# Performance work log

Measured on AMD Instinct MI355X. Metric: run time of the kernel, lower is better.

## Reference

```python
import jax, jax.numpy as jnp
import numpy as np

HEADS = 16
DIM_HEAD = 64
QUERY_DIM = 1024
CONTEXT_DIM = 1024
D_ATTN = HEADS * DIM_HEAD
SCALE = DIM_HEAD ** -0.5


def setup_inputs() -> dict:
    key = jax.random.key(0)
    ks = jax.random.split(key, 7)
    B, N, M = 4, 2048, 1024
    x = jax.random.normal(ks[0], (B, N, QUERY_DIM), dtype=jnp.float32)
    context = jax.random.normal(ks[1], (B, M, CONTEXT_DIM), dtype=jnp.float32)
    # Linear weights stored as [in, out] (no bias for Q/K/V, bias for to_out)
    s = 0.02
    Wq = jax.random.normal(ks[2], (QUERY_DIM, D_ATTN), dtype=jnp.float32) * s
    Wk = jax.random.normal(ks[3], (CONTEXT_DIM, D_ATTN), dtype=jnp.float32) * s
    Wv = jax.random.normal(ks[4], (CONTEXT_DIM, D_ATTN), dtype=jnp.float32) * s
    Wo = jax.random.normal(ks[5], (D_ATTN, QUERY_DIM), dtype=jnp.float32) * s
    bo = jax.random.normal(ks[6], (QUERY_DIM,), dtype=jnp.float32) * s
    return {"x": x, "context": context, "Wq": Wq, "Wk": Wk, "Wv": Wv, "Wo": Wo, "bo": bo}


def reference(x, context, Wq, Wk, Wv, Wo, bo):
    B, N, _ = x.shape
    M = context.shape[1]
    Q = (x @ Wq).reshape(B, N, HEADS, DIM_HEAD)        # b n h d
    K = (context @ Wk).reshape(B, M, HEADS, DIM_HEAD)  # b m h d
    V = (context @ Wv).reshape(B, M, HEADS, DIM_HEAD)
    # scores: b q h m  (matches torch einsum 'bqhd,bhmd->bqhm')
    scores = jnp.einsum('bqhd,bmhd->bqhm', Q, K) * SCALE
    attn = jax.nn.softmax(scores, axis=-1)
    out = jnp.einsum('bqhm,bmhd->bqhd', attn, V)
    out = out.reshape(B, N, D_ATTN)
    return out @ Wo + bo  # dropout p=0.0 -> identity
```

## Files before the change

kernel.cpp:

```cpp
#include <hip/hip_runtime.h>
#include <math.h>


#define HEADS 16
#define DHEAD 64
#define DM    1024
#define BQ    4
#define NQ    2048
#define MK    1024

typedef unsigned short u16;
typedef __attribute__((ext_vector_type(8))) short bf16x8;
typedef __attribute__((ext_vector_type(4))) float f32x4;
typedef __attribute__((ext_vector_type(16))) float f32x16;

__device__ __forceinline__ u16 f2bf(float f) {
  unsigned u = __builtin_bit_cast(unsigned, f);
  u = u + 0x7FFFu + ((u >> 16) & 1u);
  return (u16)(u >> 16);
}

__device__ __forceinline__ unsigned cvtpk(float lo, float hi2) {
  unsigned r;
  asm("v_cvt_pk_bf16_f32 %0, %1, %2" : "=v"(r) : "v"(lo), "v"(hi2));
  return r;
}

__device__ __forceinline__ float max3f(float a, float b, float c) {
  float d;
  asm("v_max3_f32 %0, %1, %2, %3" : "=v"(d) : "v"(a), "v"(b), "v"(c));
  return d;
}

__device__ __forceinline__ void gld16(const u16* g, u16* l) {
  __builtin_amdgcn_global_load_lds((const __attribute__((address_space(1))) void*)g,
                                   (__attribute__((address_space(3))) void*)l,
                                   16, 0, 0);
}

__global__ void k_cvt(const float* __restrict__ in, u16* __restrict__ out, int n8) {
  int i = blockIdx.x * 256 + threadIdx.x;
  if (i >= n8) return;
  float4 a = ((const float4*)in)[i * 2];
  float4 b = ((const float4*)in)[i * 2 + 1];
  union { u16 h[8]; int4 v; } r;
  r.h[0] = f2bf(a.x); r.h[1] = f2bf(a.y); r.h[2] = f2bf(a.z); r.h[3] = f2bf(a.w);
  r.h[4] = f2bf(b.x); r.h[5] = f2bf(b.y); r.h[6] = f2bf(b.z); r.h[7] = f2bf(b.w);
  ((int4*)out)[i] = r.v;
}

__global__ void k_wt(const float* __restrict__ W0, const float* __restrict__ W1,
                     const float* __restrict__ W2, const float* __restrict__ W3,
                     u16* __restrict__ out) {
  __shared__ float t[32][33];
  const float* W = blockIdx.z == 0 ? W0 : blockIdx.z == 1 ? W1 : blockIdx.z == 2 ? W2 : W3;
  u16* o = out + (size_t)blockIdx.z * DM * DM;
  int r0 = blockIdx.y * 32, c0 = blockIdx.x * 32;
  int tx = threadIdx.x, ty = threadIdx.y;
  for (int i = ty; i < 32; i += 8) t[i][tx] = W[(size_t)(r0 + i) * DM + c0 + tx];
  __syncthreads();
  for (int i = ty; i < 32; i += 8) o[(size_t)(c0 + i) * DM + r0 + tx] = f2bf(t[tx][i]);
}


#define STG2(buf, k0) do {                               \
  gld16(gA0 + (k0), &As[buf][w * 512]);                  \
  gld16(gA1 + (k0), &As[buf][4096 + w * 512]);           \
  gld16(gB0 + (k0), &Bs[buf][w * 512]);                  \
} while (0)

#define GEMM2_COMPUTE(cur) do {                                                          \
  bf16x8 af[4], bfr[4];                                                                  \
  _Pragma("unroll")                                                                      \
  for (int mi = 0; mi < 4; mi++)                                                         \
    af[mi]  = *(const bf16x8*)&As[cur][(wr * 64 + mi * 16 + lrow) * 32 + sl];            \
  _Pragma("unroll")                                                                      \
  for (int ni = 0; ni < 4; ni++)                                                         \
    bfr[ni] = *(const bf16x8*)&Bs[cur][(wc * 64 + ni * 16 + lrow) * 32 + sl];            \
  __builtin_amdgcn_s_setprio(1);                                                         \
  _Pragma("unroll")                                                                      \
  for (int mi = 0; mi < 4; mi++)                                                         \
    _Pragma("unroll")                                                                    \
    for (int ni = 0; ni < 4; ni++)                                                       \
      acc[mi][ni] = __builtin_amdgcn_mfma_f32_16x16x32_bf16(af[mi], bfr[ni],             \
                                                            acc[mi][ni], 0, 0, 0);      \
  __builtin_amdgcn_s_setprio(0);                                                         \
} while (0)

#define GEMM2_LOOP() do {                                      \
  STG2(0, 0);                                                  \
  _Pragma("unroll 2")                                          \
  for (int kt = 0; kt < 32; ++kt) {                            \
    int cur = kt & 1;                                          \
    if (kt < 31) {                                             \
      STG2(cur ^ 1, (kt + 1) * 32);                            \
      asm volatile("s_waitcnt vmcnt(3)" ::: "memory");         \
    } else {                                                   \
      asm volatile("s_waitcnt vmcnt(0)" ::: "memory");         \
    }                                                          \
    __builtin_amdgcn_s_barrier();                              \
    __builtin_amdgcn_sched_barrier(0);                         \
    GEMM2_COMPUTE(cur);                                        \
    __builtin_amdgcn_sched_barrier(0);                         \
    __builtin_amdgcn_s_barrier();                              \
    __builtin_amdgcn_sched_barrier(0);                         \
  }                                                            \
} while (0)

__global__ __launch_bounds__(512, 2) void k_gemm_qkv(const u16* __restrict__ xb,
                                                     const u16* __restrict__ cb,
                                                     const u16* __restrict__ wt,
                                                     u16* __restrict__ Qb,
                                                     u16* __restrict__ Kb,
                                                     u16* __restrict__ Vtb) {
  __shared__ u16 As[2][8192];
  __shared__ u16 Bs[2][4096];
  int lin = blockIdx.x;
  int swz = (lin & 7) * 64 + (lin >> 3);
  int p = swz >> 3, bx = swz & 7;
  const u16* A; const u16* Bt; u16* obf; int row0, mode;
  if (p < 32)      { A = xb; Bt = wt;           obf = Qb;  row0 = p * 256;        mode = 0; }
  else if (p < 48) { A = cb; Bt = wt + 1048576; obf = Kb;  row0 = (p - 32) * 256; mode = 0; }
  else             { A = cb; Bt = wt + 2097152; obf = Vtb; row0 = (p - 48) * 256; mode = 1; }
  int col0 = bx * 128;
  int t = threadIdx.x;
  int w = t >> 6, lane = t & 63, lrow = lane & 15, lgrp = lane >> 4;
  int wr = w >> 1, wc = w & 1;
  int sl = (lgrp ^ (lrow & 3)) * 8;
  f32x4 acc[4][4] = {};
  int srow = t >> 2;
  int scol = ((t & 3) ^ (srow & 3)) * 8;
  const u16* gA0 = A  + (size_t)(row0 + srow) * DM + scol;
  const u16* gA1 = gA0 + (size_t)128 * DM;
  const u16* gB0 = Bt + (size_t)(col0 + srow) * DM + scol;

  GEMM2_LOOP();

  #pragma unroll
  for (int mi = 0; mi < 4; mi++)
    #pragma unroll
    for (int ni = 0; ni < 4; ni++)
      #pragma unroll
      for (int j = 0; j < 4; j++) {
        int gr = row0 + wr * 64 + mi * 16 + lgrp * 4 + j;
        int gc = col0 + wc * 64 + ni * 16 + lrow;
        float v = acc[mi][ni][j];
        if (mode == 0) {
          obf[(size_t)gr * DM + gc] = f2bf(v);
        } else {
          int b = gr >> 10, m = gr & 1023;
          obf[((size_t)(b * DM + gc)) * MK + m] = f2bf(v);
        }
      }
}

__global__ __launch_bounds__(512, 2) void k_gemm_o(const u16* __restrict__ A,
                                                   const u16* __restrict__ Bt,
                                                   float* __restrict__ of32,
                                                   const float* __restrict__ bias) {
  __shared__ u16 As[2][8192];
  __shared__ u16 Bs[2][4096];
  int lin = blockIdx.x;
  int swz = (lin & 7) * 32 + (lin >> 3);
  int p = swz >> 3, bx = swz & 7;
  int row0 = p * 256, col0 = bx * 128;
  int t = threadIdx.x;
  int w = t >> 6, lane = t & 63, lrow = lane & 15, lgrp = lane >> 4;
  int wr = w >> 1, wc = w & 1;
  int sl = (lgrp ^ (lrow & 3)) * 8;
  f32x4 acc[4][4] = {};
  int srow = t >> 2;
  int scol = ((t & 3) ^ (srow & 3)) * 8;
  const u16* gA0 = A  + (size_t)(row0 + srow) * DM + scol;
  const u16* gA1 = gA0 + (size_t)128 * DM;
  const u16* gB0 = Bt + (size_t)(col0 + srow) * DM + scol;

  GEMM2_LOOP();

  #pragma unroll
  for (int mi = 0; mi < 4; mi++)
    #pragma unroll
    for (int ni = 0; ni < 4; ni++)
      #pragma unroll
      for (int j = 0; j < 4; j++) {
        int gr = row0 + wr * 64 + mi * 16 + lgrp * 4 + j;
        int gc = col0 + wc * 64 + ni * 16 + lrow;
        of32[(size_t)gr * DM + gc] = acc[mi][ni][j] + bias[gc];
      }
}

#define BUILD_PFRAG(sv, base, frag) {                     \
  unsigned a_ = cvtpk(sv[base + 0], sv[base + 1]);        \
  unsigned c_ = cvtpk(sv[base + 2], sv[base + 3]);        \
  unsigned b_ = cvtpk(sv[base + 4], sv[base + 5]);        \
  unsigned d_ = cvtpk(sv[base + 6], sv[base + 7]);        \
  asm("v_permlane32_swap_b32 %0, %1" : "+v"(a_), "+v"(b_)); \
  asm("v_permlane32_swap_b32 %0, %1" : "+v"(c_), "+v"(d_)); \
  union { unsigned w[4]; bf16x8 v; } u_;                  \
  u_.w[0] = a_;  u_.w[1] = c_;                            \
  u_.w[2] = b_;  u_.w[3] = d_;                            \
  frag = u_.v; }

#define PV_CHUNK(sv, base, c) {                                               \
  bf16x8 pf_; BUILD_PFRAG(sv, base, pf_);                                     \
  int mo_ = ((c) * 16 + hi * 8) ^ sw;                                         \
  bf16x8 vf0_ = *(const bf16x8*)&Vlc[ln * 64 + mo_];                          \
  bf16x8 vf1_ = *(const bf16x8*)&Vlc[(32 + ln) * 64 + mo_];                   \
  __builtin_amdgcn_s_setprio(1);                                              \
  o0 = __builtin_amdgcn_mfma_f32_32x32x16_bf16(vf0_, pf_, o0, 0, 0, 0);       \
  o1 = __builtin_amdgcn_mfma_f32_32x32x16_bf16(vf1_, pf_, o1, 0, 0, 0);       \
  __builtin_amdgcn_s_setprio(0); }

__device__ __forceinline__ float max16(const f32x16 &v) {
  float m0 = max3f(v[0], v[1], v[2]);
  float m1 = max3f(v[3], v[4], v[5]);
  float m2 = max3f(v[6], v[7], v[8]);
  float m3 = max3f(v[9], v[10], v[11]);
  float m4 = max3f(v[12], v[13], v[14]);
  float a = max3f(m0, m1, m2);
  float b = max3f(m3, m4, v[15]);
  return fmaxf(a, b);
}

__device__ __forceinline__ float sum16(const f32x16 &v) {
  float a = (v[0] + v[1]) + (v[2] + v[3]);
  float b = (v[4] + v[5]) + (v[6] + v[7]);
  float c = (v[8] + v[9]) + (v[10] + v[11]);
  float d = (v[12] + v[13]) + (v[14] + v[15]);
  return (a + b) + (c + d);
}

__global__ __launch_bounds__(512) void k_attn(const u16* __restrict__ Q,
                                              const u16* __restrict__ K,
                                              const u16* __restrict__ Vt,
                                              u16* __restrict__ O) {
  __shared__ __align__(16) u16 Kl[2][4096];
  __shared__ __align__(16) u16 Vl[2][4096];
  int bh = blockIdx.y, b = bh >> 4, h = bh & 15;
  int n0 = blockIdx.x * 256;
  int t = threadIdx.x, w = t >> 6, lane = t & 63;
  int ln = lane & 31, hi = lane >> 5;
  const float s2 = 0.18033688011112042f;

  int qrow = n0 + w * 32 + ln;
  const u16* qp = &Q[(((size_t)(b * NQ + qrow)) * HEADS + h) * DHEAD + hi * 8];
  bf16x8 qf0 = *(const bf16x8*)(qp);
  bf16x8 qf1 = *(const bf16x8*)(qp + 16);
  bf16x8 qf2 = *(const bf16x8*)(qp + 32);
  bf16x8 qf3 = *(const bf16x8*)(qp + 48);

  f32x16 o0 = {}, o1 = {};
  float M_ = -1e30f, L_ = 0.f;

  int srow = t >> 3, sp = (t & 7) * 8;
  const u16* kg = &K[(((size_t)(b * MK + srow)) * HEADS + h) * DHEAD + sp];
  const u16* vg = &Vt[((size_t)(b * DM) + h * DHEAD + srow) * MK + sp];
  int sd = srow * 64 + (sp ^ ((srow & 7) << 3));
  int sw = (ln & 7) << 3;

  int4 kv = *(const int4*)kg;
  int4 vv = *(const int4*)vg;
  *(int4*)&Kl[0][sd] = kv;
  *(int4*)&Vl[0][sd] = vv;
  __syncthreads();

  for (int it = 0; it < 16; ++it) {
    int cur = it & 1;
    const u16* Klc = Kl[cur];
    const u16* Vlc = Vl[cur];
    if (it < 15) {
      kv = *(const int4*)(kg + (size_t)(it + 1) * (64 * HEADS * DHEAD));
      vv = *(const int4*)(vg + (it + 1) * 64);
    }

    f32x16 s0 = {}, s1 = {};
    __builtin_amdgcn_s_setprio(1);
    #pragma unroll
    for (int kd = 0; kd < 4; ++kd) {
      int doff = (kd * 16 + hi * 8) ^ sw;
      bf16x8 kf0 = *(const bf16x8*)&Klc[ln * 64 + doff];
      bf16x8 kf1 = *(const bf16x8*)&Klc[(32 + ln) * 64 + doff];
      bf16x8 qk = kd == 0 ? qf0 : kd == 1 ? qf1 : kd == 2 ? qf2 : qf3;
      s0 = __builtin_amdgcn_mfma_f32_32x32x16_bf16(kf0, qk, s0, 0, 0, 0);
      s1 = __builtin_amdgcn_mfma_f32_32x32x16_bf16(kf1, qk, s1, 0, 0, 0);
    }
    __builtin_amdgcn_s_setprio(0);

    float vm = fmaxf(max16(s0), max16(s1));

    if (!__all(vm - M_ <= 8.0f)) {
      float vm2 = fmaxf(vm, __shfl_xor(vm, 32));
      float mn = fmaxf(M_, vm2);
      float rc = exp2f((M_ - mn) * s2);
      M_ = mn;
      L_ *= rc;
      #pragma unroll
      for (int i = 0; i < 16; ++i) { o0[i] *= rc; o1[i] *= rc; }
    }
    float nb = M_ * s2;
    #pragma unroll
    for (int i = 0; i < 16; ++i) s0[i] = exp2f(s0[i] * s2 - nb);
    #pragma unroll
    for (int i = 0; i < 16; ++i) s1[i] = exp2f(s1[i] * s2 - nb);
    L_ += sum16(s0) + sum16(s1);

    PV_CHUNK(s0, 0, 0);
    PV_CHUNK(s0, 8, 1);
    PV_CHUNK(s1, 0, 2);
    PV_CHUNK(s1, 8, 3);

    if (it < 15) {
      *(int4*)&Kl[cur ^ 1][sd] = kv;
      *(int4*)&Vl[cur ^ 1][sd] = vv;
    }
    __syncthreads();
  }

  float Lt = L_ + __shfl_xor(L_, 32);
  float inv = 1.0f / Lt;
  u16* ob = (u16*)&O[(((size_t)(b * NQ + qrow)) * HEADS + h) * DHEAD];
  #pragma unroll
  for (int g = 0; g < 4; ++g) {
    union { u16 h4[4]; uint2 v; } r0, r1;
    #pragma unroll
    for (int s = 0; s < 4; ++s) {
      r0.h4[s] = f2bf(o0[4 * g + s] * inv);
      r1.h4[s] = f2bf(o1[4 * g + s] * inv);
    }
    *(uint2*)(ob + 8 * g + 4 * hi) = r0.v;
    *(uint2*)(ob + 32 + 8 * g + 4 * hi) = r1.v;
  }
}

extern "C" void kernel_launch(void* const* d_in, const int* in_sizes, int n_in,
                              void* d_out, int out_size, void* d_ws, size_t ws_size,
                              hipStream_t stream) {
  (void)in_sizes; (void)n_in; (void)out_size; (void)ws_size;
  const float* x   = (const float*)d_in[0];
  const float* ctx = (const float*)d_in[1];
  const float* Wq  = (const float*)d_in[2];
  const float* Wk  = (const float*)d_in[3];
  const float* Wv  = (const float*)d_in[4];
  const float* Wo  = (const float*)d_in[5];
  const float* bo  = (const float*)d_in[6];
  float* out = (float*)d_out;
  char* ws = (char*)d_ws;
  const size_t MB = 1u << 20;
  u16* xb  = (u16*)(ws);
  u16* cb  = (u16*)(ws + 16 * MB);
  u16* wt  = (u16*)(ws + 24 * MB);
  u16* Qb  = (u16*)(ws + 32 * MB);
  u16* Kb  = (u16*)(ws + 48 * MB);
  u16* Vtb = (u16*)(ws + 56 * MB);
  u16* Ab  = (u16*)(ws + 64 * MB);

  k_cvt<<<4096, 256, 0, stream>>>(x,   xb, 1048576);
  k_cvt<<<2048, 256, 0, stream>>>(ctx, cb, 524288);
  k_wt<<<dim3(32, 32, 4), dim3(32, 8), 0, stream>>>(Wq, Wk, Wv, Wo, wt);

  k_gemm_qkv<<<512, 512, 0, stream>>>(xb, cb, wt, Qb, Kb, Vtb);

  k_attn<<<dim3(8, 64), 512, 0, stream>>>(Qb, Kb, Vtb, Ab);

  k_gemm_o<<<256, 512, 0, stream>>>(Ab, wt + 3145728, out, bo);
}
```

Before: 175.6 us.

## Retile GEMMs to 128x128 with 256 threads, fold softmax scale into Q, MFMA row sums

```diff
diff --git a/kernel.cpp b/kernel.cpp
--- a/kernel.cpp
+++ b/kernel.cpp
@@ -11,6 +11,7 @@
 
 typedef unsigned short u16;
 typedef __attribute__((ext_vector_type(8))) short bf16x8;
+typedef __attribute__((ext_vector_type(2))) float f32x2;
 typedef __attribute__((ext_vector_type(4))) float f32x4;
 typedef __attribute__((ext_vector_type(16))) float f32x16;
 
@@ -29,6 +30,23 @@
 __device__ __forceinline__ float max3f(float a, float b, float c) {
   float d;
   asm("v_max3_f32 %0, %1, %2, %3" : "=v"(d) : "v"(a), "v"(b), "v"(c));
+  return d;
+}
+
+__device__ __forceinline__ float fexp2(float x) {
+  float r;
+  asm("v_exp_f32 %0, %1" : "=v"(r) : "v"(x));
+  return r;
+}
+
+__device__ __forceinline__ f32x2 pk_add(f32x2 a, f32x2 b) {
+  f32x2 d;
+  asm("v_pk_add_f32 %0, %1, %2" : "=v"(d) : "v"(a), "v"(b));
+  return d;
+}
+__device__ __forceinline__ f32x2 pk_mul(f32x2 a, f32x2 b) {
+  f32x2 d;
+  asm("v_pk_mul_f32 %0, %1, %2" : "=v"(d) : "v"(a), "v"(b));
   return d;
 }
 
@@ -63,88 +81,86 @@
 }
 
 
-#define STG2(buf, k0) do {                               \
-  gld16(gA0 + (k0), &As[buf][w * 512]);                  \
-  gld16(gA1 + (k0), &As[buf][4096 + w * 512]);           \
-  gld16(gB0 + (k0), &Bs[buf][w * 512]);                  \
+#define G97_STG(buf, k0) do {                                    \
+  gld16(gA0 + (k0), &As[buf][w * 512]);                          \
+  gld16(gA1 + (k0), &As[buf][2048 + w * 512]);                   \
+  gld16(gB0 + (k0), &Bs[buf][w * 512]);                          \
+  gld16(gB1 + (k0), &Bs[buf][2048 + w * 512]);                   \
 } while (0)
 
-#define GEMM2_COMPUTE(cur) do {                                                          \
-  bf16x8 af[4], bfr[4];                                                                  \
-  _Pragma("unroll")                                                                      \
-  for (int mi = 0; mi < 4; mi++)                                                         \
-    af[mi]  = *(const bf16x8*)&As[cur][(wr * 64 + mi * 16 + lrow) * 32 + sl];            \
-  _Pragma("unroll")                                                                      \
-  for (int ni = 0; ni < 4; ni++)                                                         \
-    bfr[ni] = *(const bf16x8*)&Bs[cur][(wc * 64 + ni * 16 + lrow) * 32 + sl];            \
-  __builtin_amdgcn_s_setprio(1);                                                         \
-  _Pragma("unroll")                                                                      \
-  for (int mi = 0; mi < 4; mi++)                                                         \
-    _Pragma("unroll")                                                                    \
-    for (int ni = 0; ni < 4; ni++)                                                       \
-      acc[mi][ni] = __builtin_amdgcn_mfma_f32_16x16x32_bf16(af[mi], bfr[ni],             \
-                                                            acc[mi][ni], 0, 0, 0);      \
-  __builtin_amdgcn_s_setprio(0);                                                         \
+#define G97_LOOP() do {                                                        \
+  G97_STG(0, 0);                                                               \
+  _Pragma("unroll 2")                                                          \
+  for (int kt = 0; kt < 32; ++kt) {                                            \
+    int cur = kt & 1;                                                          \
+    if (kt < 31) {                                                             \
+      G97_STG(cur ^ 1, (kt + 1) * 32);                                         \
+      asm volatile("s_waitcnt vmcnt(4)" ::: "memory");                         \
+    } else {                                                                   \
+      asm volatile("s_waitcnt vmcnt(0)" ::: "memory");                         \
+    }                                                                          \
+    __builtin_amdgcn_s_barrier();                                              \
+    bf16x8 af[4], bfr[4];                                                      \
+    _Pragma("unroll")                                                          \
+    for (int mi = 0; mi < 4; ++mi)                                             \
+      af[mi]  = *(const bf16x8*)&As[cur][(wr * 64 + mi * 16 + lrow) * 32 + fo]; \
+    _Pragma("unroll")                                                          \
+    for (int ni = 0; ni < 4; ++ni)                                             \
+      bfr[ni] = *(const bf16x8*)&Bs[cur][(wc * 64 + ni * 16 + lrow) * 32 + fo]; \
+    __builtin_amdgcn_s_setprio(1);                                             \
+    _Pragma("unroll")                                                          \
+    for (int mi = 0; mi < 4; ++mi)                                             \
+      _Pragma("unroll")                                                        \
+      for (int ni = 0; ni < 4; ++ni)                                           \
+        acc[mi][ni] = __builtin_amdgcn_mfma_f32_16x16x32_bf16(af[mi], bfr[ni], \
+                                                              acc[mi][ni], 0, 0, 0); \
+    __builtin_amdgcn_s_setprio(0);                                             \
+    __builtin_amdgcn_s_barrier();                                              \
+  }                                                                            \
 } while (0)
 
-#define GEMM2_LOOP() do {                                      \
-  STG2(0, 0);                                                  \
-  _Pragma("unroll 2")                                          \
-  for (int kt = 0; kt < 32; ++kt) {                            \
-    int cur = kt & 1;                                          \
-    if (kt < 31) {                                             \
-      STG2(cur ^ 1, (kt + 1) * 32);                            \
-      asm volatile("s_waitcnt vmcnt(3)" ::: "memory");         \
-    } else {                                                   \
-      asm volatile("s_waitcnt vmcnt(0)" ::: "memory");         \
-    }                                                          \
-    __builtin_amdgcn_s_barrier();                              \
-    __builtin_amdgcn_sched_barrier(0);                         \
-    GEMM2_COMPUTE(cur);                                        \
-    __builtin_amdgcn_sched_barrier(0);                         \
-    __builtin_amdgcn_s_barrier();                              \
-    __builtin_amdgcn_sched_barrier(0);                         \
-  }                                                            \
-} while (0)
-
-__global__ __launch_bounds__(512, 2) void k_gemm_qkv(const u16* __restrict__ xb,
+#define G97_SETUP()                                                            \
+  int t = threadIdx.x;                                                         \
+  int w = t >> 6, lane = t & 63, lrow = lane & 15, lgrp = lane >> 4;           \
+  int wr = w >> 1, wc = w & 1;                                                 \
+  int fo = (lgrp ^ ((lrow >> 1) & 3)) * 8;                                     \
+  int srow = t >> 2, su = ((t & 3) ^ ((srow >> 1) & 3)) * 8;                   \
+  f32x4 acc[4][4] = {};
+
+__global__ __launch_bounds__(256, 3) void k_gemm_qkv(const u16* __restrict__ xb,
                                                      const u16* __restrict__ cb,
                                                      const u16* __restrict__ wt,
                                                      u16* __restrict__ Qb,
                                                      u16* __restrict__ Kb,
                                                      u16* __restrict__ Vtb) {
-  __shared__ u16 As[2][8192];
+  __shared__ u16 As[2][4096];
   __shared__ u16 Bs[2][4096];
   int lin = blockIdx.x;
-  int swz = (lin & 7) * 64 + (lin >> 3);
+  int swz = (lin & 7) * 128 + (lin >> 3);
   int p = swz >> 3, bx = swz & 7;
   const u16* A; const u16* Bt; u16* obf; int row0, mode;
-  if (p < 32)      { A = xb; Bt = wt;           obf = Qb;  row0 = p * 256;        mode = 0; }
-  else if (p < 48) { A = cb; Bt = wt + 1048576; obf = Kb;  row0 = (p - 32) * 256; mode = 0; }
-  else             { A = cb; Bt = wt + 2097152; obf = Vtb; row0 = (p - 48) * 256; mode = 1; }
+  float osc;
+  if (p < 64)      { A = xb; Bt = wt;           obf = Qb;  row0 = p * 128;        mode = 0; osc = 0.18033688011112042f; }
+  else if (p < 96) { A = cb; Bt = wt + 1048576; obf = Kb;  row0 = (p - 64) * 128; mode = 0; osc = 1.0f; }
+  else             { A = cb; Bt = wt + 2097152; obf = Vtb; row0 = (p - 96) * 128; mode = 1; osc = 1.0f; }
   int col0 = bx * 128;
-  int t = threadIdx.x;
-  int w = t >> 6, lane = t & 63, lrow = lane & 15, lgrp = lane >> 4;
-  int wr = w >> 1, wc = w & 1;
-  int sl = (lgrp ^ (lrow & 3)) * 8;
-  f32x4 acc[4][4] = {};
-  int srow = t >> 2;
-  int scol = ((t & 3) ^ (srow & 3)) * 8;
-  const u16* gA0 = A  + (size_t)(row0 + srow) * DM + scol;
-  const u16* gA1 = gA0 + (size_t)128 * DM;
-  const u16* gB0 = Bt + (size_t)(col0 + srow) * DM + scol;
-
-  GEMM2_LOOP();
+  G97_SETUP();
+  const u16* gA0 = A  + (size_t)(row0 + srow) * DM + su;
+  const u16* gA1 = gA0 + (size_t)64 * DM;
+  const u16* gB0 = Bt + (size_t)(col0 + srow) * DM + su;
+  const u16* gB1 = gB0 + (size_t)64 * DM;
+
+  G97_LOOP();
 
   #pragma unroll
-  for (int mi = 0; mi < 4; mi++)
-    #pragma unroll
-    for (int ni = 0; ni < 4; ni++)
+  for (int mi = 0; mi < 4; ++mi)
+    #pragma unroll
+    for (int ni = 0; ni < 4; ++ni)
       #pragma unroll
-      for (int j = 0; j < 4; j++) {
+      for (int j = 0; j < 4; ++j) {
         int gr = row0 + wr * 64 + mi * 16 + lgrp * 4 + j;
         int gc = col0 + wc * 64 + ni * 16 + lrow;
-        float v = acc[mi][ni][j];
+        float v = acc[mi][ni][j] * osc;
         if (mode == 0) {
           obf[(size_t)gr * DM + gc] = f2bf(v);
         } else {
@@ -154,35 +170,30 @@
       }
 }
 
-__global__ __launch_bounds__(512, 2) void k_gemm_o(const u16* __restrict__ A,
+__global__ __launch_bounds__(256, 3) void k_gemm_o(const u16* __restrict__ A,
                                                    const u16* __restrict__ Bt,
                                                    float* __restrict__ of32,
                                                    const float* __restrict__ bias) {
-  __shared__ u16 As[2][8192];
+  __shared__ u16 As[2][4096];
   __shared__ u16 Bs[2][4096];
   int lin = blockIdx.x;
-  int swz = (lin & 7) * 32 + (lin >> 3);
+  int swz = (lin & 7) * 64 + (lin >> 3);
   int p = swz >> 3, bx = swz & 7;
-  int row0 = p * 256, col0 = bx * 128;
-  int t = threadIdx.x;
-  int w = t >> 6, lane = t & 63, lrow = lane & 15, lgrp = lane >> 4;
-  int wr = w >> 1, wc = w & 1;
-  int sl = (lgrp ^ (lrow & 3)) * 8;
-  f32x4 acc[4][4] = {};
-  int srow = t >> 2;
-  int scol = ((t & 3) ^ (srow & 3)) * 8;
-  const u16* gA0 = A  + (size_t)(row0 + srow) * DM + scol;
-  const u16* gA1 = gA0 + (size_t)128 * DM;
-  const u16* gB0 = Bt + (size_t)(col0 + srow) * DM + scol;
-
-  GEMM2_LOOP();
+  int row0 = p * 128, col0 = bx * 128;
+  G97_SETUP();
+  const u16* gA0 = A  + (size_t)(row0 + srow) * DM + su;
+  const u16* gA1 = gA0 + (size_t)64 * DM;
+  const u16* gB0 = Bt + (size_t)(col0 + srow) * DM + su;
+  const u16* gB1 = gB0 + (size_t)64 * DM;
+
+  G97_LOOP();
 
   #pragma unroll
-  for (int mi = 0; mi < 4; mi++)
-    #pragma unroll
-    for (int ni = 0; ni < 4; ni++)
+  for (int mi = 0; mi < 4; ++mi)
+    #pragma unroll
+    for (int ni = 0; ni < 4; ++ni)
       #pragma unroll
-      for (int j = 0; j < 4; j++) {
+      for (int j = 0; j < 4; ++j) {
         int gr = row0 + wr * 64 + mi * 16 + lgrp * 4 + j;
         int gc = col0 + wc * 64 + ni * 16 + lrow;
         of32[(size_t)gr * DM + gc] = acc[mi][ni][j] + bias[gc];
@@ -204,11 +215,12 @@
 #define PV_CHUNK(sv, base, c) {                                               \
   bf16x8 pf_; BUILD_PFRAG(sv, base, pf_);                                     \
   int mo_ = ((c) * 16 + hi * 8) ^ sw;                                         \
-  bf16x8 vf0_ = *(const bf16x8*)&Vlc[ln * 64 + mo_];                          \
-  bf16x8 vf1_ = *(const bf16x8*)&Vlc[(32 + ln) * 64 + mo_];                   \
+  bf16x8 vf0_ = *(const bf16x8*)&Vl[cur][ln * 64 + mo_];                      \
+  bf16x8 vf1_ = *(const bf16x8*)&Vl[cur][(32 + ln) * 64 + mo_];               \
   __builtin_amdgcn_s_setprio(1);                                              \
   o0 = __builtin_amdgcn_mfma_f32_32x32x16_bf16(vf0_, pf_, o0, 0, 0, 0);       \
   o1 = __builtin_amdgcn_mfma_f32_32x32x16_bf16(vf1_, pf_, o1, 0, 0, 0);       \
+  Lacc = __builtin_amdgcn_mfma_f32_32x32x16_bf16(onesf, pf_, Lacc, 0, 0, 0);  \
   __builtin_amdgcn_s_setprio(0); }
 
 __device__ __forceinline__ float max16(const f32x16 &v) {
@@ -222,25 +234,19 @@
   return fmaxf(a, b);
 }
 
-__device__ __forceinline__ float sum16(const f32x16 &v) {
-  float a = (v[0] + v[1]) + (v[2] + v[3]);
-  float b = (v[4] + v[5]) + (v[6] + v[7]);
-  float c = (v[8] + v[9]) + (v[10] + v[11]);
-  float d = (v[12] + v[13]) + (v[14] + v[15]);
-  return (a + b) + (c + d);
-}
-
 __global__ __launch_bounds__(512) void k_attn(const u16* __restrict__ Q,
                                               const u16* __restrict__ K,
                                               const u16* __restrict__ Vt,
                                               u16* __restrict__ O) {
   __shared__ __align__(16) u16 Kl[2][4096];
   __shared__ __align__(16) u16 Vl[2][4096];
-  int bh = blockIdx.y, b = bh >> 4, h = bh & 15;
-  int n0 = blockIdx.x * 256;
+  int wgid = blockIdx.x;
+  int bh = (wgid & 7) * 8 + (wgid >> 6);
+  int nt = (wgid >> 3) & 7;
+  int b = bh >> 4, h = bh & 15;
+  int n0 = nt * 256;
   int t = threadIdx.x, w = t >> 6, lane = t & 63;
   int ln = lane & 31, hi = lane >> 5;
-  const float s2 = 0.18033688011112042f;
 
   int qrow = n0 + w * 32 + ln;
   const u16* qp = &Q[(((size_t)(b * NQ + qrow)) * HEADS + h) * DHEAD + hi * 8];
@@ -249,8 +255,11 @@
   bf16x8 qf2 = *(const bf16x8*)(qp + 32);
   bf16x8 qf3 = *(const bf16x8*)(qp + 48);
 
-  f32x16 o0 = {}, o1 = {};
-  float M_ = -1e30f, L_ = 0.f;
+  const short one_ = (short)0x3F80;
+  bf16x8 onesf = {one_, one_, one_, one_, one_, one_, one_, one_};
+
+  f32x16 o0 = {}, o1 = {}, Lacc = {};
+  float M_ = -1e30f;
 
   int srow = t >> 3, sp = (t & 7) * 8;
   const u16* kg = &K[(((size_t)(b * MK + srow)) * HEADS + h) * DHEAD + sp];
@@ -266,8 +275,6 @@
 
   for (int it = 0; it < 16; ++it) {
     int cur = it & 1;
-    const u16* Klc = Kl[cur];
-    const u16* Vlc = Vl[cur];
     if (it < 15) {
       kv = *(const int4*)(kg + (size_t)(it + 1) * (64 * HEADS * DHEAD));
       vv = *(const int4*)(vg + (it + 1) * 64);
@@ -278,8 +285,8 @@
     #pragma unroll
     for (int kd = 0; kd < 4; ++kd) {
       int doff = (kd * 16 + hi * 8) ^ sw;
-      bf16x8 kf0 = *(const bf16x8*)&Klc[ln * 64 + doff];
-      bf16x8 kf1 = *(const bf16x8*)&Klc[(32 + ln) * 64 + doff];
+      bf16x8 kf0 = *(const bf16x8*)&Kl[cur][ln * 64 + doff];
+      bf16x8 kf1 = *(const bf16x8*)&Kl[cur][(32 + ln) * 64 + doff];
       bf16x8 qk = kd == 0 ? qf0 : kd == 1 ? qf1 : kd == 2 ? qf2 : qf3;
       s0 = __builtin_amdgcn_mfma_f32_32x32x16_bf16(kf0, qk, s0, 0, 0, 0);
       s1 = __builtin_amdgcn_mfma_f32_32x32x16_bf16(kf1, qk, s1, 0, 0, 0);
@@ -288,21 +295,31 @@
 
     float vm = fmaxf(max16(s0), max16(s1));
 
-    if (!__all(vm - M_ <= 8.0f)) {
+    if (!__all(vm - M_ <= 1.44269504f)) {
       float vm2 = fmaxf(vm, __shfl_xor(vm, 32));
       float mn = fmaxf(M_, vm2);
-      float rc = exp2f((M_ - mn) * s2);
+      float rc = fexp2(M_ - mn);
       M_ = mn;
-      L_ *= rc;
+      Lacc[0] *= rc;
+      f32x2 rc2 = {rc, rc};
+      f32x2* o0p = (f32x2*)&o0;
+      f32x2* o1p = (f32x2*)&o1;
       #pragma unroll
-      for (int i = 0; i < 16; ++i) { o0[i] *= rc; o1[i] *= rc; }
-    }
-    float nb = M_ * s2;
-    #pragma unroll
-    for (int i = 0; i < 16; ++i) s0[i] = exp2f(s0[i] * s2 - nb);
-    #pragma unroll
-    for (int i = 0; i < 16; ++i) s1[i] = exp2f(s1[i] * s2 - nb);
-    L_ += sum16(s0) + sum16(s1);
+      for (int i = 0; i < 8; ++i) { o0p[i] = pk_mul(o0p[i], rc2); }
+      #pragma unroll
+      for (int i = 0; i < 8; ++i) { o1p[i] = pk_mul(o1p[i], rc2); }
+    }
+    f32x2 nb2 = {-M_, -M_};
+    f32x2* s0p = (f32x2*)&s0;
+    f32x2* s1p = (f32x2*)&s1;
+    #pragma unroll
+    for (int i = 0; i < 8; ++i) s0p[i] = pk_add(s0p[i], nb2);
+    #pragma unroll
+    for (int i = 0; i < 8; ++i) s1p[i] = pk_add(s1p[i], nb2);
+    #pragma unroll
+    for (int i = 0; i < 16; ++i) s0[i] = fexp2(s0[i]);
+    #pragma unroll
+    for (int i = 0; i < 16; ++i) s1[i] = fexp2(s1[i]);
 
     PV_CHUNK(s0, 0, 0);
     PV_CHUNK(s0, 8, 1);
@@ -316,8 +333,7 @@
     __syncthreads();
   }
 
-  float Lt = L_ + __shfl_xor(L_, 32);
-  float inv = 1.0f / Lt;
+  float inv = 1.0f / Lacc[0];
   u16* ob = (u16*)&O[(((size_t)(b * NQ + qrow)) * HEADS + h) * DHEAD];
   #pragma unroll
   for (int g = 0; g < 4; ++g) {
@@ -358,9 +374,9 @@
   k_cvt<<<2048, 256, 0, stream>>>(ctx, cb, 524288);
   k_wt<<<dim3(32, 32, 4), dim3(32, 8), 0, stream>>>(Wq, Wk, Wv, Wo, wt);
 
-  k_gemm_qkv<<<512, 512, 0, stream>>>(xb, cb, wt, Qb, Kb, Vtb);
-
-  k_attn<<<dim3(8, 64), 512, 0, stream>>>(Qb, Kb, Vtb, Ab);
-
-  k_gemm_o<<<256, 512, 0, stream>>>(Ab, wt + 3145728, out, bo);
-}
+  k_gemm_qkv<<<1024, 256, 0, stream>>>(xb, cb, wt, Qb, Kb, Vtb);
+
+  k_attn<<<512, 512, 0, stream>>>(Qb, Kb, Vtb, Ab);
+
+  k_gemm_o<<<512, 256, 0, stream>>>(Ab, wt + 3145728, out, bo);
+}
```

Result: faster. 162.5 us (-7.5%).
